# Kernel tuning notes

Hardware: AMD Instinct MI355X
Metric: run time of the kernel (lower is better)

Reference implementation:

```python
import jax, jax.numpy as jnp
import numpy as np

B, Q, E = 32768, 1024, 1024  # batch, quant_dim, embed_dim


def setup_inputs() -> dict:
    key = jax.random.key(0)
    k1, k2, k3, k4, k5 = jax.random.split(key, 5)
    s = lambda n: 1.0 / np.sqrt(n)
    x = jax.random.normal(k1, (B, Q), jnp.float32)
    # nn.Linear weights, shape [out_features, in_features]
    W1 = jax.random.normal(k2, (2 * Q, Q), jnp.float32) * s(Q)      # selector layer 1
    W2 = jax.random.normal(k3, (Q, 2 * Q), jnp.float32) * s(2 * Q)  # selector layer 2
    W3 = jax.random.normal(k4, (Q, Q), jnp.float32) * s(Q)          # selector layer 3
    Wc = jax.random.normal(k5, (E, Q), jnp.float32) * s(Q)          # codebook
    return {"x": x, "W1": W1, "W2": W2, "W3": W3, "Wc": Wc}


def dyn_k_hot(x, k_scores):
    # k per row = argmax(k_scores) + 1
    k_values = jnp.argmax(k_scores, axis=-1, keepdims=True) + 1  # [B,1]
    # torch: sorted_indices = argsort(x, descending); mask gathered by argsort(sorted_indices)
    # equivalently: rank of each element in descending order < k
    ranks = jnp.argsort(jnp.argsort(-x, axis=-1), axis=-1)       # [B,Q]
    return (ranks < k_values).astype(x.dtype)


def reference(x, W1, W2, W3, Wc):
    # dynkselector: Linear -> ReLU -> Linear -> ReLU -> Linear (no biases)
    h = jax.nn.relu(x @ W1.T)
    h = jax.nn.relu(h @ W2.T)
    k_scores = h @ W3.T
    k_hot = dyn_k_hot(x, k_scores)   # [B,Q] {0,1}
    return k_hot @ Wc.T              # codebook projection -> [B,E]
```

## Files before the change

### kernel.cpp

```cpp
#include <hip/hip_runtime.h>
#include <stdint.h>

#define B_  32768
#define Q_  1024
#define E_  1024
#define CAPF  4096
#define CAPF2 1024

typedef __attribute__((ext_vector_type(8))) short bf16x8;
typedef __attribute__((ext_vector_type(8))) _Float16 f16x8;
typedef __attribute__((ext_vector_type(8))) unsigned short u16x8;
typedef __attribute__((ext_vector_type(4))) float f32x4;
typedef unsigned short us;

__device__ __forceinline__ f32x4 MFMA16(bf16x8 a, bf16x8 b, f32x4 c) {
    return __builtin_amdgcn_mfma_f32_16x16x32_bf16(a, b, c, 0, 0, 0);
}
__device__ __forceinline__ f32x4 MFMA16H(bf16x8 a, bf16x8 b, f32x4 c) {
    return __builtin_amdgcn_mfma_f32_16x16x32_f16(
        __builtin_bit_cast(f16x8, a), __builtin_bit_cast(f16x8, b), c, 0, 0, 0);
}

__device__ __forceinline__ us f2bf(float v) {
    unsigned u = __float_as_uint(v);
    u += 0x7FFFu + ((u >> 16) & 1u);
    return (us)(u >> 16);
}
__device__ __forceinline__ float bf2f(us b) {
    return __uint_as_float(((unsigned)b) << 16);
}
__device__ __forceinline__ us f2h(float v) {
    _Float16 h = (_Float16)v;
    return __builtin_bit_cast(unsigned short, h);
}

__global__ __launch_bounds__(256)
void cvt4_h(const float* __restrict__ s0, us* __restrict__ d0, int e0,
            const float* __restrict__ s1, us* __restrict__ d1, int e1,
            const float* __restrict__ s2, us* __restrict__ d2, int e2,
            const float* __restrict__ s3, us* __restrict__ d3, int e3) {
    int i = blockIdx.x * 256 + threadIdx.x;
    const int stride = gridDim.x * 256;
    for (; i < e3; i += stride) {
        const float* s; us* d; int j;
        if (i < e0)      { s = s0; d = d0; j = i; }
        else if (i < e1) { s = s1; d = d1; j = i - e0; }
        else if (i < e2) { s = s2; d = d2; j = i - e1; }
        else             { s = s3; d = d3; j = i - e2; }
        float4 a = ((const float4*)s)[j * 2];
        float4 b = ((const float4*)s)[j * 2 + 1];
        float f[8] = {a.x, a.y, a.z, a.w, b.x, b.y, b.z, b.w};
        u16x8 h;
#pragma unroll
        for (int k = 0; k < 8; ++k) h[k] = f2h(f[k]);
        ((u16x8*)d)[j] = h;
    }
}

__global__ __launch_bounds__(256)
void split3_k(const float* __restrict__ s0, us* __restrict__ h0, us* __restrict__ l0, int e0,
              const float* __restrict__ s1, us* __restrict__ h1, us* __restrict__ l1, int e1,
              const float* __restrict__ s2, us* __restrict__ h2, us* __restrict__ l2, int e2) {
    int i = blockIdx.x * 256 + threadIdx.x;
    const int stride = gridDim.x * 256;
    for (; i < e2; i += stride) {
        const float* s; us *dh, *dl; int j;
        if (i < e0)      { s = s0; dh = h0; dl = l0; j = i; }
        else if (i < e1) { s = s1; dh = h1; dl = l1; j = i - e0; }
        else             { s = s2; dh = h2; dl = l2; j = i - e1; }
        float4 a = ((const float4*)s)[j * 2];
        float4 b = ((const float4*)s)[j * 2 + 1];
        float f[8] = {a.x, a.y, a.z, a.w, b.x, b.y, b.z, b.w};
        u16x8 h, l;
#pragma unroll
        for (int k = 0; k < 8; ++k) {
            us c0 = f2bf(f[k]);
            h[k] = c0;
            l[k] = f2bf(f[k] - bf2f(c0));
        }
        ((u16x8*)dh)[j] = h;
        ((u16x8*)dl)[j] = l;
    }
}

__global__ __launch_bounds__(256)
void cvt_plane_k(const float* __restrict__ in, us* __restrict__ hi, int n8) {
    int i = blockIdx.x * 256 + threadIdx.x;
    const int stride = gridDim.x * 256;
    for (; i < n8; i += stride) {
        float4 a = ((const float4*)in)[i * 2];
        float4 b = ((const float4*)in)[i * 2 + 1];
        float f[8] = {a.x, a.y, a.z, a.w, b.x, b.y, b.z, b.w};
        u16x8 h;
#pragma unroll
        for (int j = 0; j < 8; ++j) h[j] = f2bf(f[j]);
        ((u16x8*)hi)[i] = h;
    }
}

__global__ __launch_bounds__(256)
void gather_split(const float* __restrict__ X, const int* __restrict__ flags,
                  const int* __restrict__ cnt, us* __restrict__ G0,
                  us* __restrict__ G1) {
    const int n = min(*cnt, CAPF);
    for (int it = blockIdx.x; it < n; it += gridDim.x) {
        int row = flags[it];
        if ((unsigned)row >= B_) row = 0;
        float4 v = ((const float4*)(X + (size_t)row * Q_))[threadIdx.x];
        float f[4] = {v.x, v.y, v.z, v.w};
        us h[4], l[4];
#pragma unroll
        for (int j = 0; j < 4; ++j) {
            h[j] = f2bf(f[j]);
            l[j] = f2bf(f[j] - bf2f(h[j]));
        }
        *(uint2*)&G0[(size_t)it * Q_ + threadIdx.x * 4] = *(uint2*)h;
        *(uint2*)&G1[(size_t)it * Q_ + threadIdx.x * 4] = *(uint2*)l;
    }
}

template<int SPLITS, int MODE>
__global__ __launch_bounds__(256)
void finalize_k(const float* __restrict__ P, size_t pstride,
                us* __restrict__ o0, us* __restrict__ o1,
                float* __restrict__ of, const int* __restrict__ cnt, int N) {
    const int n = min(*cnt, CAPF);
    const int total4 = n * (N >> 2);
    int i = blockIdx.x * 256 + threadIdx.x;
    const int stride = gridDim.x * 256;
    for (; i < total4; i += stride) {
        float4 s = ((const float4*)P)[i];
#pragma unroll
        for (int sp = 1; sp < SPLITS; ++sp) {
            float4 p = *(const float4*)(P + (size_t)sp * pstride + (size_t)i * 4);
            s.x += p.x; s.y += p.y; s.z += p.z; s.w += p.w;
        }
        if constexpr (MODE == 0) {
            ((float4*)of)[i] = s;
        } else {
            float f[4] = {fmaxf(s.x, 0.f), fmaxf(s.y, 0.f),
                          fmaxf(s.z, 0.f), fmaxf(s.w, 0.f)};
            us h[4], l[4];
#pragma unroll
            for (int j = 0; j < 4; ++j) {
                h[j] = f2bf(f[j]);
                l[j] = f2bf(f[j] - bf2f(h[j]));
            }
            *(uint2*)&o0[(size_t)i * 4] = *(uint2*)h;
            *(uint2*)&o1[(size_t)i * 4] = *(uint2*)l;
        }
    }
}

#define LGKM0() asm volatile("s_waitcnt lgkmcnt(0)" ::: "memory")
#define VMC8()  asm volatile("s_waitcnt vmcnt(8)" ::: "memory")
#define BAR()   __builtin_amdgcn_s_barrier()
#define RD_AB(Aarr, Barr, slot) { \
    const us* _la = &LA[(slot) * 8192]; const us* _lb = &LB[(slot) * 8192]; \
    _Pragma("unroll") for (int mf = 0; mf < 8; ++mf) Aarr[mf] = *(const bf16x8*)&_la[ago[mf]]; \
    _Pragma("unroll") for (int nf = 0; nf < 4; ++nf) Barr[nf] = *(const bf16x8*)&_lb[bgo[nf]]; }
#define CLX(AF, BF) { __builtin_amdgcn_s_setprio(1); \
    _Pragma("unroll") for (int mf = 0; mf < 8; ++mf) { \
        _Pragma("unroll") for (int nf = 0; nf < 4; ++nf) { \
            if constexpr (FP16) acc[mf][nf] = MFMA16H(AF[mf], BF[nf], acc[mf][nf]); \
            else               acc[mf][nf] = MFMA16 (AF[mf], BF[nf], acc[mf][nf]); } } \
    __builtin_amdgcn_s_setprio(0); }

template<int NSEG, int K, int EMIT, bool RELU, bool FP16>
__global__ __launch_bounds__(512, 2)
void gemm4r(const us* __restrict__ A0p, const us* __restrict__ A1p,
            const us* __restrict__ B0p, const us* __restrict__ B1p,
            void* __restrict__ Cp0, void* __restrict__ Cp1, int N) {
    constexpr int TPS = K / 32;
    constexpr int NT  = NSEG * TPS;
    static_assert(NT % 2 == 0 && NT >= 4, "shape");
    __shared__ __align__(16) us LA[4 * 8192];
    __shared__ __align__(16) us LB[4 * 8192];

    const int t = threadIdx.x;
    const int wv = t >> 6, lane = t & 63;
    const int lanelo = lane & 15, kq = lane >> 4;
    const int wm = wv >> 2, wn = wv & 3;

    const int q8 = gridDim.x >> 3;
    const int logical = ((int)blockIdx.x & 7) * q8 + ((int)blockIdx.x >> 3);
    const int gx = N >> 8;
    const int m0 = (logical / gx) * 256, n0 = (logical % gx) * 256;

    int soff[2], ldst[2];
#pragma unroll
    for (int i = 0; i < 2; ++i) {
        int s = i * 512 + t;
        int row = s >> 2, c = s & 3;
        soff[i] = row * K + (c ^ ((row >> 1) & 3)) * 8;
        ldst[i] = (i * 512 + wv * 64) * 8;
    }
    int ago[8], bgo[4];
#pragma unroll
    for (int mf = 0; mf < 8; ++mf) {
        int row = wm * 128 + mf * 16 + lanelo;
        ago[mf] = (row * 4 + (kq ^ ((row >> 1) & 3))) * 8;
    }
#pragma unroll
    for (int nf = 0; nf < 4; ++nf) {
        int row = wn * 64 + nf * 16 + lanelo;
        bgo[nf] = (row * 4 + (kq ^ ((row >> 1) & 3))) * 8;
    }

    auto stage = [&](int tv) {
        int slot = tv & 3;
        int seg = tv / TPS;
        int kb  = (tv - seg * TPS) * 32;
        const us* Ap = (NSEG == 1 || seg < 2) ? A0p : A1p;
        const us* Bp = (NSEG == 3 && seg == 1) ? B1p : B0p;
        const us* Abase = Ap + (size_t)m0 * K + kb;
        const us* Bbase = Bp + (size_t)n0 * K + kb;
        us* dA = &LA[slot * 8192];
        us* dB = &LB[slot * 8192];
#pragma unroll
        for (int i = 0; i < 2; ++i) {
            __builtin_amdgcn_global_load_lds(
                (const __attribute__((address_space(1))) void*)(Abase + soff[i]),
                (__attribute__((address_space(3))) void*)(dA + ldst[i]), 16, 0, 0);
            __builtin_amdgcn_global_load_lds(
                (const __attribute__((address_space(1))) void*)(Bbase + soff[i]),
                (__attribute__((address_space(3))) void*)(dB + ldst[i]), 16, 0, 0);
        }
    };

    f32x4 acc[8][4];
#pragma unroll
    for (int i = 0; i < 8; ++i)
#pragma unroll
        for (int j = 0; j < 4; ++j) acc[i][j] = (f32x4){0.f, 0.f, 0.f, 0.f};

    bf16x8 aE[8], bE[4], aO[8], bO[4];

    stage(0); stage(1); stage(2);
    VMC8();  BAR();
    RD_AB(aE, bE, 0);
    stage(3);
    LGKM0(); VMC8(); BAR();

    for (int tt = 0; tt < NT; tt += 2) {
        RD_AB(aO, bO, (tt + 1) & 3);
        { int tv = tt + 4; if (tv > NT - 1) tv = NT - 1; stage(tv); }
        CLX(aE, bE);
        LGKM0(); VMC8(); BAR();
        { int tn = (tt + 2 < NT) ? (tt + 2) : (NT - 1);
          RD_AB(aE, bE, tn & 3); }
        { int tv = tt + 5; if (tv > NT - 1) tv = NT - 1; stage(tv); }
        CLX(aO, bO);
        LGKM0(); VMC8(); BAR();
    }

#pragma unroll
    for (int mf = 0; mf < 8; ++mf)
#pragma unroll
        for (int nf = 0; nf < 4; ++nf)
#pragma unroll
            for (int r = 0; r < 4; ++r) {
                int row = m0 + wm * 128 + mf * 16 + kq * 4 + r;
                int col = n0 + wn * 64 + nf * 16 + lanelo;
                float v = acc[mf][nf][r];
                if constexpr (RELU) v = fmaxf(v, 0.f);
                if constexpr (EMIT == 1) {
                    us c0 = f2bf(v);
                    ((us*)Cp0)[(size_t)row * N + col] = c0;
                    ((us*)Cp1)[(size_t)row * N + col] = f2bf(v - bf2f(c0));
                } else if constexpr (EMIT == 2) {
                    ((us*)Cp0)[(size_t)row * N + col] = f2h(v);
                } else {
                    ((float*)Cp0)[(size_t)row * N + col] = v;
                }
            }
}

template<int NPASS, int SPLITS>
__global__ __launch_bounds__(256, 4)
void gemm_sp(const us* __restrict__ A0, const us* __restrict__ A1,
             const us* __restrict__ B0, const us* __restrict__ B1,
             float* __restrict__ P, size_t pstride,
             int N, int K, const int* __restrict__ ncnt) {
    __shared__ __align__(16) us A0s[128 * 32];
    __shared__ __align__(16) us B0s[128 * 32];

    const int t = threadIdx.x;
    const int wave = t >> 6, lane = t & 63;
    const int lanelo = lane & 15, kq = lane >> 4;
    const int wm = wave >> 1, wn = wave & 1;
    const int q8 = gridDim.x >> 3;
    const int logical = ((int)blockIdx.x & 7) * q8 + ((int)blockIdx.x >> 3);
    const int gx = N >> 7;
    const int m0 = (logical / gx) * 128, n0 = (logical % gx) * 128;
    const int split = blockIdx.y;

    int nn = *ncnt; if (nn > CAPF) nn = CAPF;
    if (m0 >= ((nn + 127) & ~127)) return;

    const int Ks = K / SPLITS;
    const int kbase = split * Ks;
    const int tps = Ks >> 5;

    f32x4 acc[4][4];
#pragma unroll
    for (int i = 0; i < 4; ++i)
#pragma unroll
        for (int j = 0; j < 4; ++j) acc[i][j] = (f32x4){0.f, 0.f, 0.f, 0.f};

    for (int vt = 0; vt < NPASS * tps; ++vt) {
        const int seg = vt / tps;
        const int kt  = kbase + (vt - seg * tps) * 32;
        const us* Ap = (NPASS == 1 || seg < 2) ? A0 : A1;
        const us* Bp = (NPASS == 3 && seg == 1) ? B1 : B0;
        __syncthreads();
#pragma unroll
        for (int g = 0; g < 2; ++g) {
            int c = (g * 4 + wave) * 64 + lane;
            int row = c >> 2;
            int koff = (c & 3) ^ ((row >> 1) & 3);
            size_t offa = (size_t)(m0 + row) * K + kt + koff * 8;
            size_t offb = (size_t)(n0 + row) * K + kt + koff * 8;
            int dst = (g * 4 + wave) * 512;
            __builtin_amdgcn_global_load_lds(
                (const __attribute__((address_space(1))) void*)(Ap + offa),
                (__attribute__((address_space(3))) void*)&A0s[dst], 16, 0, 0);
            __builtin_amdgcn_global_load_lds(
                (const __attribute__((address_space(1))) void*)(Bp + offb),
                (__attribute__((address_space(3))) void*)&B0s[dst], 16, 0, 0);
        }
        __syncthreads();

        bf16x8 a0[4];
#pragma unroll
        for (int mf = 0; mf < 4; ++mf) {
            int ar = wm * 64 + mf * 16 + lanelo;
            int ac = ar * 4 + (kq ^ ((ar >> 1) & 3));
            a0[mf] = *(const bf16x8*)&A0s[ac * 8];
        }
#pragma unroll
        for (int nf = 0; nf < 4; ++nf) {
            int br = wn * 64 + nf * 16 + lanelo;
            int bc = br * 4 + (kq ^ ((br >> 1) & 3));
            bf16x8 vb0 = *(const bf16x8*)&B0s[bc * 8];
#pragma unroll
            for (int mf = 0; mf < 4; ++mf) acc[mf][nf] = MFMA16(a0[mf], vb0, acc[mf][nf]);
        }
    }

    float* Pd = P + (size_t)split * pstride;
#pragma unroll
    for (int mf = 0; mf < 4; ++mf)
#pragma unroll
        for (int nf = 0; nf < 4; ++nf)
#pragma unroll
            for (int r = 0; r < 4; ++r) {
                int row = m0 + wm * 64 + mf * 16 + kq * 4 + r;
                int col = n0 + wn * 64 + nf * 16 + lanelo;
                Pd[(size_t)row * N + col] = acc[mf][nf][r];
            }
}

__device__ __forceinline__ int chunk_of(int row, int koff) {
    return row * 4 + (koff ^ (row & 3));
}

template<int NPASS>
__device__ __forceinline__ void split_store(us* S0, us* S1,
                                            int rowX, int koffX, float4 a, float4 b) {
    int ch = chunk_of(rowX, koffX);
    float f[8] = {a.x, a.y, a.z, a.w, b.x, b.y, b.z, b.w};
    bf16x8 lo, hi;
#pragma unroll
    for (int j = 0; j < 8; ++j) {
        us c0 = f2bf(f[j]);
        lo[j] = (short)c0;
        hi[j] = (short)f2bf(f[j] - bf2f(c0));
    }
    *(bf16x8*)&S0[ch * 8] = lo;
    if constexpr (NPASS == 3) *(bf16x8*)&S1[ch * 8] = hi;
}

template<int NPASS, bool AF32, bool RELU, bool EMITP>
__global__ __launch_bounds__(256, 2)
void gemm3p(const void* __restrict__ Ap0, const void* __restrict__ Ap1,
            const float* __restrict__ Wf,
            void* __restrict__ Cp0, void* __restrict__ Cp1,
            int M, int N, int K) {
    __shared__ __align__(16) us A0s[128 * 32];
    __shared__ __align__(16) us B0s[128 * 32];
    __shared__ __align__(16) us A1s[(NPASS == 3) ? 128 * 32 : 8];
    __shared__ __align__(16) us B1s[(NPASS == 3) ? 128 * 32 : 8];

    const int t = threadIdx.x;
    const int wave = t >> 6, lane = t & 63;
    const int lanelo = lane & 15, kq = lane >> 4;
    const int wm = wave >> 1, wn = wave & 1;
    const int m0 = blockIdx.y * 128, n0 = blockIdx.x * 128;
    const int brow = t >> 1, bhalf = t & 1;

    f32x4 acc[4][4];
#pragma unroll
    for (int i = 0; i < 4; ++i)
#pragma unroll
        for (int j = 0; j < 4; ++j) acc[i][j] = (f32x4){0.f, 0.f, 0.f, 0.f};

    for (int kt = 0; kt < K; kt += 32) {
        __syncthreads();
        const float* wp = Wf + (size_t)(n0 + brow) * K + kt + bhalf * 16;
        float4 v0 = *(const float4*)(wp + 0);
        float4 v1 = *(const float4*)(wp + 4);
        float4 v2 = *(const float4*)(wp + 8);
        float4 v3 = *(const float4*)(wp + 12);
        if constexpr (AF32) {
            const float* ap = (const float*)Ap0 + (size_t)(m0 + brow) * K + kt + bhalf * 16;
            float4 u0 = *(const float4*)(ap + 0);
            float4 u1 = *(const float4*)(ap + 4);
            float4 u2 = *(const float4*)(ap + 8);
            float4 u3 = *(const float4*)(ap + 12);
            split_store<NPASS>(A0s, A1s, brow, bhalf * 2 + 0, u0, u1);
            split_store<NPASS>(A0s, A1s, brow, bhalf * 2 + 1, u2, u3);
        } else {
#pragma unroll
            for (int g = 0; g < 2; ++g) {
                int c = (g * 4 + wave) * 64 + lane;
                int row = c >> 2;
                int koff = (c & 3) ^ (row & 3);
                const us* s0 = (const us*)Ap0 + (size_t)(m0 + row) * K + kt + koff * 8;
                __builtin_amdgcn_global_load_lds(
                    (const __attribute__((address_space(1))) void*)s0,
                    (__attribute__((address_space(3))) void*)&A0s[(size_t)(g * 4 + wave) * 512],
                    16, 0, 0);
                if constexpr (NPASS == 3) {
                    const us* s1 = (const us*)Ap1 + (size_t)(m0 + row) * K + kt + koff * 8;
                    __builtin_amdgcn_global_load_lds(
                        (const __attribute__((address_space(1))) void*)s1,
                        (__attribute__((address_space(3))) void*)&A1s[(size_t)(g * 4 + wave) * 512],
                        16, 0, 0);
                }
            }
        }
        split_store<NPASS>(B0s, B1s, brow, bhalf * 2 + 0, v0, v1);
        split_store<NPASS>(B0s, B1s, brow, bhalf * 2 + 1, v2, v3);
        __syncthreads();

        bf16x8 a0[4], a1[4];
#pragma unroll
        for (int mf = 0; mf < 4; ++mf) {
            int ar = wm * 64 + mf * 16 + lanelo;
            int ac = chunk_of(ar, kq);
            a0[mf] = *(const bf16x8*)&A0s[ac * 8];
            if constexpr (NPASS == 3) a1[mf] = *(const bf16x8*)&A1s[ac * 8];
        }
#pragma unroll
        for (int nf = 0; nf < 4; ++nf) {
            int br = wn * 64 + nf * 16 + lanelo;
            int bc = chunk_of(br, kq);
            bf16x8 vb0 = *(const bf16x8*)&B0s[bc * 8];
#pragma unroll
            for (int mf = 0; mf < 4; ++mf) acc[mf][nf] = MFMA16(a0[mf], vb0, acc[mf][nf]);
            if constexpr (NPASS == 3) {
                bf16x8 vb1 = *(const bf16x8*)&B1s[bc * 8];
#pragma unroll
                for (int mf = 0; mf < 4; ++mf) acc[mf][nf] = MFMA16(a0[mf], vb1, acc[mf][nf]);
#pragma unroll
                for (int mf = 0; mf < 4; ++mf) acc[mf][nf] = MFMA16(a1[mf], vb0, acc[mf][nf]);
            }
        }
    }

#pragma unroll
    for (int mf = 0; mf < 4; ++mf)
#pragma unroll
        for (int nf = 0; nf < 4; ++nf)
#pragma unroll
            for (int r = 0; r < 4; ++r) {
                int row = m0 + wm * 64 + mf * 16 + kq * 4 + r;
                int col = n0 + wn * 64 + nf * 16 + lanelo;
                float v = acc[mf][nf][r];
                if constexpr (RELU) v = fmaxf(v, 0.f);
                if constexpr (EMITP) {
                    us c0 = f2bf(v);
                    ((us*)Cp0)[(size_t)row * N + col] = c0;
                    ((us*)Cp1)[(size_t)row * N + col] = f2bf(v - bf2f(c0));
                } else {
                    ((float*)Cp0)[(size_t)row * N + col] = v;
                }
            }
}

__global__ __launch_bounds__(256)
void row_argmax_flag(const float* __restrict__ S, int* __restrict__ KV,
                     int* __restrict__ flags, int* __restrict__ cnt, float theta) {
    int row = blockIdx.x * 4 + (threadIdx.x >> 6);
    int lane = threadIdx.x & 63;
    const float* s = S + (size_t)row * Q_;
    float b1 = -3.4e38f, b2 = -3.4e38f; int i1 = 0;
    for (int j = lane; j < Q_; j += 64) {
        float v = s[j];
        if (v > b1) { b2 = b1; b1 = v; i1 = j; }
        else if (v > b2) b2 = v;
    }
#pragma unroll
    for (int m = 1; m < 64; m <<= 1) {
        float o1 = __shfl_xor(b1, m);
        int   oi = __shfl_xor(i1, m);
        float o2 = __shfl_xor(b2, m);
        if (o1 > b1 || (o1 == b1 && oi < i1)) {
            b2 = fmaxf(b1, o2);
            b1 = o1; i1 = oi;
        } else {
            b2 = fmaxf(b2, o1);
        }
    }
    if (lane == 0) {
        KV[row] = i1 + 1;
        if (b1 - b2 < theta) {
            int p = atomicAdd(cnt, 1);
            if (p < CAPF) flags[p] = row;
        }
    }
}

__global__ __launch_bounds__(256)
void g_argmax_flag2(const float* __restrict__ SCg, const int* __restrict__ flags,
                    const int* __restrict__ cnt, int* __restrict__ KV,
                    int* __restrict__ flags2, int* __restrict__ cnt2) {
    const int lane = threadIdx.x & 63, wv = threadIdx.x >> 6;
    const int n = min(*cnt, CAPF);
    for (int it = blockIdx.x * 4 + wv; it < n; it += gridDim.x * 4) {
        const float* s = SCg + (size_t)it * Q_;
        float b1 = -3.4e38f, b2 = -3.4e38f; int i1 = 0;
        for (int j = lane; j < Q_; j += 64) {
            float v = s[j];
            if (v > b1) { b2 = b1; b1 = v; i1 = j; }
            else if (v > b2) b2 = v;
        }
#pragma unroll
        for (int m = 1; m < 64; m <<= 1) {
            float o1 = __shfl_xor(b1, m);
            int   oi = __shfl_xor(i1, m);
            float o2 = __shfl_xor(b2, m);
            if (o1 > b1 || (o1 == b1 && oi < i1)) {
                b2 = fmaxf(b1, o2);
                b1 = o1; i1 = oi;
            } else {
                b2 = fmaxf(b2, o1);
            }
        }
        if (lane == 0) {
            int r = flags[it];
            if ((unsigned)r < B_) {
                KV[r] = i1 + 1;
                if (b1 - b2 < 1e-3f) {
                    int p = atomicAdd(cnt2, 1);
                    if (p < CAPF2) flags2[p] = r;
                }
            }
        }
    }
}

template<int K, bool IN_BY_FLAG, bool RELU>
__global__ __launch_bounds__(256)
void rescore_gemm(const float* __restrict__ IN, const float* __restrict__ W,
                  float* __restrict__ OUT, const int* __restrict__ flags,
                  const int* __restrict__ cnt, int N, int cap) {
    __shared__ float xr[K];
    const int t = threadIdx.x, lane = t & 63, wv = t >> 6;
    const int n = min(*cnt, cap);
    const int chunks = N >> 4;
    for (int w = blockIdx.x; w < n * chunks; w += gridDim.x) {
        const int it = w / chunks, ch = w - it * chunks;
        int srow = IN_BY_FLAG ? flags[it] : it;
        if (IN_BY_FLAG && (unsigned)srow >= B_) srow = 0;
        const float* rp = IN + (size_t)srow * K;
        __syncthreads();
#pragma unroll
        for (int p = t; p < K / 4; p += 256)
            ((float4*)xr)[p] = ((const float4*)rp)[p];
        __syncthreads();
#pragma unroll
        for (int jj = 0; jj < 4; ++jj) {
            const int col = ch * 16 + wv * 4 + jj;
            const float* wr = W + (size_t)col * K;
            double a0 = 0.0, a1 = 0.0;
#pragma unroll
            for (int i = 0; i < K / 256; ++i) {
                const int k = i * 256 + lane * 4;
                float4 w4 = *(const float4*)(wr + k);
                float4 x4 = *(const float4*)(xr + k);
                a0 += (double)x4.x * w4.x + (double)x4.y * w4.y;
                a1 += (double)x4.z * w4.z + (double)x4.w * w4.w;
            }
            double a = a0 + a1;
#pragma unroll
            for (int m = 1; m < 64; m <<= 1) a += __shfl_xor(a, m);
            if (lane == 0) {
                float v = (float)a;
                if (RELU) v = fmaxf(v, 0.f);
                OUT[(size_t)it * N + col] = v;
            }
        }
    }
}

__global__ __launch_bounds__(256)
void rescore_argmax(const float* __restrict__ SCF, const int* __restrict__ flags,
                    const int* __restrict__ cnt, int* __restrict__ KV, int cap) {
    const int lane = threadIdx.x & 63, wv = threadIdx.x >> 6;
    const int n = min(*cnt, cap);
    for (int it = blockIdx.x * 4 + wv; it < n; it += gridDim.x * 4) {
        const float* s = SCF + (size_t)it * Q_;
        float best = -3.4e38f; int bi = 0;
        for (int j = lane; j < Q_; j += 64) {
            float v = s[j];
            if (v > best) { best = v; bi = j; }
        }
#pragma unroll
        for (int m = 1; m < 64; m <<= 1) {
            float ov = __shfl_xor(best, m); int oi = __shfl_xor(bi, m);
            if (ov > best || (ov == best && oi < bi)) { best = ov; bi = oi; }
        }
        if (lane == 0) {
            int r = flags[it];
            if ((unsigned)r < B_) KV[r] = bi + 1;
        }
    }
}

__global__ __launch_bounds__(256)
void topk_mask_radix(const float* __restrict__ X, const int* __restrict__ KV,
                     us* __restrict__ Mout) {
    const int row  = blockIdx.x * 4 + (threadIdx.x >> 6);
    const int lane = threadIdx.x & 63;
    const float* x = X + (size_t)row * Q_;

    unsigned u[16];
#pragma unroll
    for (int j4 = 0; j4 < 4; ++j4) {
        float4 v = *(const float4*)(x + lane * 16 + j4 * 4);
        float f[4] = {v.x, v.y, v.z, v.w};
#pragma unroll
        for (int e = 0; e < 4; ++e) {
            unsigned fb = __float_as_uint(f[e]);
            u[j4 * 4 + e] = (fb & 0x80000000u) ? ~fb : (fb | 0x80000000u);
        }
    }
    const int k = KV[row];

    unsigned p = 0;
#pragma unroll
    for (int b = 31; b >= 0; --b) {
        unsigned q = p | (1u << b);
        int c = 0;
#pragma unroll
        for (int j = 0; j < 16; ++j) c += (u[j] >= q);
#pragma unroll
        for (int m = 1; m < 64; m <<= 1) c += __shfl_xor(c, m);
        if (c >= k) p = q;
    }

    int gt = 0, eqloc = 0;
#pragma unroll
    for (int j = 0; j < 16; ++j) { gt += (u[j] > p); eqloc += (u[j] == p); }
    int gtot = gt;
#pragma unroll
    for (int m = 1; m < 64; m <<= 1) gtot += __shfl_xor(gtot, m);
    int scan = eqloc;
#pragma unroll
    for (int d = 1; d < 64; d <<= 1) {
        int o = __shfl_up(scan, d);
        if (lane >= d) scan += o;
    }
    int run = scan - eqloc;
    const int quota = k - gtot;

    us m16[16];
#pragma unroll
    for (int j = 0; j < 16; ++j) {
        bool one;
        if (u[j] > p) one = true;
        else if (u[j] == p) { one = (run < quota); ++run; }
        else one = false;
        m16[j] = one ? (us)0x3F80 : (us)0;
    }
    u16x8* dst = (u16x8*)(Mout + (size_t)row * Q_ + lane * 16);
    dst[0] = *(u16x8*)&m16[0];
    dst[1] = *(u16x8*)&m16[8];
}

extern "C" void kernel_launch(void* const* d_in, const int* in_sizes, int n_in,
                              void* d_out, int out_size, void* d_ws, size_t ws_size,
                              hipStream_t stream) {
    const float* x  = (const float*)d_in[0];
    const float* W1 = (const float*)d_in[1];
    const float* W2 = (const float*)d_in[2];
    const float* W3 = (const float*)d_in[3];
    const float* Wc = (const float*)d_in[4];
    float* out = (float*)d_out;

    char* ws = (char*)d_ws;
    char* dob = (char*)d_out;
    us*    H1f  = (us*)ws;
    float* SC   = (float*)(ws + ((size_t)128 << 20));
    float* P1   = (float*)ws;
    us*    H1g0 = (us*)(ws + ((size_t)128 << 20));
    us*    H1g1 = (us*)(ws + ((size_t)144 << 20));
    us*    H2g0 = (us*)(ws + ((size_t)160 << 20));
    us*    H2g1 = (us*)(ws + ((size_t)168 << 20));
    float* SCg  = (float*)(ws + ((size_t)176 << 20));
    us*    MASKB= (us*)(ws + ((size_t)192 << 20));
    int* KV     = (int*)(ws + ((size_t)256 << 20));
    int* FLAGS  = KV + B_;
    int* CNT    = FLAGS + B_;
    int* CNT2   = CNT + 1;
    int* FLAGS2 = CNT2 + 1;
    us*    Xf   = (us*)dob;
    us*    H2f  = (us*)(dob + ((size_t)64 << 20));
    us*    Xg0  = (us*)dob;
    us*    Xg1  = (us*)(dob + ((size_t)32 << 20));
    float* P23  = (float*)(dob + ((size_t)64 << 20));
    float* H1F  = (float*)dob;
    float* H2F  = (float*)(dob + ((size_t)8 << 20));
    float* SCF  = (float*)(dob + ((size_t)12 << 20));
    char* WP = ws + ((size_t)256 << 20) + ((size_t)512 << 10);
    us* W1h = (us*)WP;                       us* W1f = (us*)WP;
    us* W1l = W1h + (size_t)2 * Q_ * Q_;
    us* W2h = W1l + (size_t)2 * Q_ * Q_;     us* W2f = W1l;
    us* W2l = W2h + (size_t)2 * Q_ * Q_;
    us* W3h = W2l + (size_t)2 * Q_ * Q_;     us* W3f = W2h;
    us* W3l = W3h + (size_t)Q_ * Q_;
    us* Wch = W3l + (size_t)Q_ * Q_;
    const size_t NEEDED = ((size_t)256 << 20) + ((size_t)512 << 10) + ((size_t)22 << 20);

    const size_t PS1 = (size_t)CAPF * 2 * Q_;
    const size_t PS2 = (size_t)CAPF * Q_;

    hipMemsetAsync(CNT, 0, 2 * sizeof(int), stream);
    dim3 blk(256);

    if (ws_size >= NEEDED) {
        const int ex  = B_ * Q_ / 8;
        const int ew1 = ex + 2 * Q_ * Q_ / 8;
        const int ew2 = ew1 + 2 * Q_ * Q_ / 8;
        const int ew3 = ew2 + Q_ * Q_ / 8;
        cvt4_h<<<dim3(2048), blk, 0, stream>>>(x, Xf, ex, W1, W1f, ew1,
                                               W2, W2f, ew2, W3, W3f, ew3);
        gemm4r<1, Q_,     2, true,  true ><<<dim3(1024), dim3(512), 0, stream>>>(
            Xf,  nullptr, W1f, nullptr, H1f, nullptr, 2 * Q_);
        gemm4r<1, 2 * Q_, 2, true,  true ><<<dim3(512),  dim3(512), 0, stream>>>(
            H1f, nullptr, W2f, nullptr, H2f, nullptr, Q_);
        gemm4r<1, Q_,     0, false, true ><<<dim3(512),  dim3(512), 0, stream>>>(
            H2f, nullptr, W3f, nullptr, SC,  nullptr, Q_);
        row_argmax_flag<<<dim3(B_ / 4), blk, 0, stream>>>(SC, KV, FLAGS, CNT, 0.008f);
        const int es1 = 2 * Q_ * Q_ / 8;
        const int es2 = es1 + 2 * Q_ * Q_ / 8;
        const int es3 = es2 + Q_ * Q_ / 8;
        split3_k<<<dim3(1024), blk, 0, stream>>>(W1, W1h, W1l, es1,
                                                 W2, W2h, W2l, es2,
                                                 W3, W3h, W3l, es3);
        cvt_plane_k<<<dim3(512), blk, 0, stream>>>(Wc, Wch, E_ * Q_ / 8);
        gather_split<<<dim3(2048), blk, 0, stream>>>(x, FLAGS, CNT, Xg0, Xg1);
        gemm_sp<3, 4><<<dim3((CAPF / 128) * (2 * Q_ / 128), 4), blk, 0, stream>>>(
            Xg0,  Xg1,  W1h, W1l, P1,  PS1, 2 * Q_, Q_, CNT);
        finalize_k<4, 1><<<dim3(2048), blk, 0, stream>>>(P1,  PS1, H1g0, H1g1, nullptr, CNT, 2 * Q_);
        gemm_sp<3, 4><<<dim3((CAPF / 128) * (Q_ / 128), 4), blk, 0, stream>>>(
            H1g0, H1g1, W2h, W2l, P23, PS2, Q_, 2 * Q_, CNT);
        finalize_k<4, 1><<<dim3(2048), blk, 0, stream>>>(P23, PS2, H2g0, H2g1, nullptr, CNT, Q_);
        gemm_sp<3, 4><<<dim3((CAPF / 128) * (Q_ / 128), 4), blk, 0, stream>>>(
            H2g0, H2g1, W3h, W3l, P23, PS2, Q_, Q_, CNT);
        finalize_k<4, 0><<<dim3(2048), blk, 0, stream>>>(P23, PS2, nullptr, nullptr, SCg, CNT, Q_);
        g_argmax_flag2<<<dim3(1024), blk, 0, stream>>>(SCg, FLAGS, CNT, KV, FLAGS2, CNT2);
        rescore_gemm<Q_,     true,  true ><<<dim3(4096), blk, 0, stream>>>(x,   W1, H1F, FLAGS2, CNT2, 2 * Q_, CAPF2);
        rescore_gemm<2 * Q_, false, true ><<<dim3(2048), blk, 0, stream>>>(H1F, W2, H2F, FLAGS2, CNT2, Q_,     CAPF2);
        rescore_gemm<Q_,     false, false><<<dim3(2048), blk, 0, stream>>>(H2F, W3, SCF, FLAGS2, CNT2, Q_,     CAPF2);
        rescore_argmax<<<dim3(64), blk, 0, stream>>>(SCF, FLAGS2, CNT2, KV, CAPF2);
        topk_mask_radix<<<dim3(B_ / 4), blk, 0, stream>>>(x, KV, MASKB);
        gemm4r<1, Q_, 0, false, false><<<dim3(512), dim3(512), 0, stream>>>(
            MASKB, nullptr, Wch, nullptr, out, nullptr, E_);
    } else {
        us*    H1_0 = (us*)ws;
        us*    H1_1 = (us*)(ws + ((size_t)128 << 20));
        float* SCo  = (float*)ws;
        us*    MB   = (us*)(ws + ((size_t)128 << 20));
        us* H2_0 = (us*)d_out;
        us* H2_1 = (us*)d_out + (size_t)B_ * Q_;
        float* H1Fo = (float*)ws;
        float* H2Fo = (float*)(ws + ((size_t)128 << 20));
        float* SCFo = (float*)(ws + ((size_t)192 << 20));
        gemm3p<3, true,  true,  true ><<<dim3(2 * Q_ / 128, B_ / 128), blk, 0, stream>>>(
            x, nullptr, W1, H1_0, H1_1, B_, 2 * Q_, Q_);
        gemm3p<3, false, true,  true ><<<dim3(Q_ / 128, B_ / 128), blk, 0, stream>>>(
            H1_0, H1_1, W2, H2_0, H2_1, B_, Q_, 2 * Q_);
        gemm3p<3, false, false, false><<<dim3(Q_ / 128, B_ / 128), blk, 0, stream>>>(
            H2_0, H2_1, W3, SCo, nullptr, B_, Q_, Q_);
        row_argmax_flag<<<dim3(B_ / 4), blk, 0, stream>>>(SCo, KV, FLAGS, CNT, 1e-3f);
        rescore_gemm<Q_,     true,  true ><<<dim3(4096), blk, 0, stream>>>(x,    W1, H1Fo, FLAGS, CNT, 2 * Q_, CAPF);
        rescore_gemm<2 * Q_, false, true ><<<dim3(2048), blk, 0, stream>>>(H1Fo, W2, H2Fo, FLAGS, CNT, Q_,     CAPF);
        rescore_gemm<Q_,     false, false><<<dim3(2048), blk, 0, stream>>>(H2Fo, W3, SCFo, FLAGS, CNT, Q_,     CAPF);
        rescore_argmax<<<dim3(64), blk, 0, stream>>>(SCFo, FLAGS, CNT, KV, CAPF);
        topk_mask_radix<<<dim3(B_ / 4), blk, 0, stream>>>(x, KV, MB);
        gemm3p<1, false, false, false><<<dim3(E_ / 128, B_ / 128), blk, 0, stream>>>(
            MB, nullptr, Wc, out, nullptr, B_, E_, Q_);
    }
}
```

Measured before the change: 1.064 ms.

## Fuse row argmax and top-2 margin into third GEMM epilogue

The third selector GEMM no longer writes the full fp32 score matrix. Its epilogue computes a per-tile top-1/top-2 and argmax through shuffles and LDS, then writes one small float4 per row per column tile. A light merge kernel combines the tiles to produce k values and flag ambiguous rows. This removes a 128MB score write and re-read. In exchange it adds epilogue reduction work, an extra barrier and a vmcnt(0) drain.

```diff
diff --git a/kernel.cpp b/kernel.cpp
--- a/kernel.cpp
+++ b/kernel.cpp
@@ -152,8 +152,31 @@
     }
 }
 
+__global__ __launch_bounds__(256)
+void argmax_merge(const float4* __restrict__ PT, int gx, int* __restrict__ KV,
+                  int* __restrict__ flags, int* __restrict__ cnt, float theta) {
+    const int row = blockIdx.x * 256 + threadIdx.x;
+    float b1 = -3.4e38f, b2 = -3.4e38f; int i1 = 0;
+    for (int ti = 0; ti < gx; ++ti) {
+        float4 e = PT[(size_t)row * gx + ti];
+        float o1 = e.x, o2 = e.y; int oi = __float_as_int(e.z);
+        if (o1 > b1 || (o1 == b1 && oi < i1)) {
+            b2 = fmaxf(b1, o2);
+            b1 = o1; i1 = oi;
+        } else {
+            b2 = fmaxf(b2, o1);
+        }
+    }
+    KV[row] = i1 + 1;
+    if (b1 - b2 < theta) {
+        int p = atomicAdd(cnt, 1);
+        if (p < CAPF) flags[p] = row;
+    }
+}
+
 #define LGKM0() asm volatile("s_waitcnt lgkmcnt(0)" ::: "memory")
 #define VMC8()  asm volatile("s_waitcnt vmcnt(8)" ::: "memory")
+#define VMC0A() asm volatile("s_waitcnt vmcnt(0)" ::: "memory")
 #define BAR()   __builtin_amdgcn_s_barrier()
 #define RD_AB(Aarr, Barr, slot) { \
     const us* _la = &LA[(slot) * 8192]; const us* _lb = &LB[(slot) * 8192]; \
@@ -252,6 +275,61 @@
         { int tv = tt + 5; if (tv > NT - 1) tv = NT - 1; stage(tv); }
         CLX(aO, bO);
         LGKM0(); VMC8(); BAR();
+    }
+
+    if constexpr (EMIT == 3) {
+        VMC0A(); BAR();
+        float* SD = (float*)LA;
+#pragma unroll
+        for (int mf = 0; mf < 8; ++mf)
+#pragma unroll
+            for (int r = 0; r < 4; ++r) {
+                float b1 = -3.4e38f, b2 = -3.4e38f; int i1 = 0;
+#pragma unroll
+                for (int nf = 0; nf < 4; ++nf) {
+                    float v = acc[mf][nf][r];
+                    int c = wn * 64 + nf * 16 + lanelo;
+                    if (v > b1 || (v == b1 && c < i1)) { b2 = b1; b1 = v; i1 = c; }
+                    else if (v > b2) b2 = v;
+                }
+#pragma unroll
+                for (int m = 1; m < 16; m <<= 1) {
+                    float o1 = __shfl_xor(b1, m);
+                    int   oi = __shfl_xor(i1, m);
+                    float o2 = __shfl_xor(b2, m);
+                    if (o1 > b1 || (o1 == b1 && oi < i1)) {
+                        b2 = fmaxf(b1, o2);
+                        b1 = o1; i1 = oi;
+                    } else {
+                        b2 = fmaxf(b2, o1);
+                    }
+                }
+                if (lanelo == 0) {
+                    int rl = wm * 128 + mf * 16 + kq * 4 + r;
+                    SD[(rl * 4 + wn) * 4 + 0] = b1;
+                    SD[(rl * 4 + wn) * 4 + 1] = b2;
+                    SD[(rl * 4 + wn) * 4 + 2] = __int_as_float(i1);
+                }
+            }
+        BAR();
+        if (t < 256) {
+            float b1 = -3.4e38f, b2 = -3.4e38f; int i1 = 0;
+#pragma unroll
+            for (int w2 = 0; w2 < 4; ++w2) {
+                float o1 = SD[(t * 4 + w2) * 4 + 0];
+                float o2 = SD[(t * 4 + w2) * 4 + 1];
+                int   oi = __float_as_int(SD[(t * 4 + w2) * 4 + 2]);
+                if (o1 > b1 || (o1 == b1 && oi < i1)) {
+                    b2 = fmaxf(b1, o2);
+                    b1 = o1; i1 = oi;
+                } else {
+                    b2 = fmaxf(b2, o1);
+                }
+            }
+            float4 e; e.x = b1; e.y = b2; e.z = __int_as_float(n0 + i1); e.w = 0.f;
+            ((float4*)Cp0)[(size_t)(m0 + t) * gx + (n0 >> 8)] = e;
+        }
+        return;
     }
 
 #pragma unroll
@@ -703,13 +781,13 @@
     char* ws = (char*)d_ws;
     char* dob = (char*)d_out;
     us*    H1f  = (us*)ws;
-    float* SC   = (float*)(ws + ((size_t)128 << 20));
     float* P1   = (float*)ws;
     us*    H1g0 = (us*)(ws + ((size_t)128 << 20));
     us*    H1g1 = (us*)(ws + ((size_t)144 << 20));
     us*    H2g0 = (us*)(ws + ((size_t)160 << 20));
     us*    H2g1 = (us*)(ws + ((size_t)168 << 20));
     float* SCg  = (float*)(ws + ((size_t)176 << 20));
+    float4* PT  = (float4*)(ws + ((size_t)176 << 20));
     us*    MASKB= (us*)(ws + ((size_t)192 << 20));
     int* KV     = (int*)(ws + ((size_t)256 << 20));
     int* FLAGS  = KV + B_;
@@ -751,9 +829,9 @@
             Xf,  nullptr, W1f, nullptr, H1f, nullptr, 2 * Q_);
         gemm4r<1, 2 * Q_, 2, true,  true ><<<dim3(512),  dim3(512), 0, stream>>>(
             H1f, nullptr, W2f, nullptr, H2f, nullptr, Q_);
-        gemm4r<1, Q_,     0, false, true ><<<dim3(512),  dim3(512), 0, stream>>>(
-            H2f, nullptr, W3f, nullptr, SC,  nullptr, Q_);
-        row_argmax_flag<<<dim3(B_ / 4), blk, 0, stream>>>(SC, KV, FLAGS, CNT, 0.008f);
+        gemm4r<1, Q_,     3, false, true ><<<dim3(512),  dim3(512), 0, stream>>>(
+            H2f, nullptr, W3f, nullptr, PT,  nullptr, Q_);
+        argmax_merge<<<dim3(B_ / 256), blk, 0, stream>>>(PT, Q_ >> 8, KV, FLAGS, CNT, 0.008f);
         const int es1 = 2 * Q_ * Q_ / 8;
         const int es2 = es1 + 2 * Q_ * Q_ / 8;
         const int es3 = es2 + Q_ * Q_ / 8;
```

New measurement: 1.051 ms. No clear change (-1.2%).
